# Kernel tuning notes

Hardware: AMD Instinct MI355X
Metric: run time of the kernel (lower is better)

## Reference

```python
import jax, jax.numpy as jnp
import numpy as np

N = 100000   # nodes
E = 600000   # edges per relation
D = 128      # input_dim == output_dim, num_heads = 1
NEG_SLOPE = 0.2  # DGL GATConv default leaky_relu slope


def setup_inputs() -> dict:
    key = jax.random.key(0)
    ks = jax.random.split(key, 10)
    scale = 1.0 / np.sqrt(D)
    return {
        "feat_src": jax.random.normal(ks[0], (N, D), jnp.float32) * 0.1,
        "feat_dst": jax.random.normal(ks[1], (N, D), jnp.float32) * 0.1,
        "intra_src": jax.random.randint(ks[2], (E,), 0, N, jnp.int32),
        "intra_dst": jax.random.randint(ks[3], (E,), 0, N, jnp.int32),
        "inter_src": jax.random.randint(ks[4], (E,), 0, N, jnp.int32),
        "inter_dst": jax.random.randint(ks[5], (E,), 0, N, jnp.int32),
        # 8 GATConvs: conv{1..4} x {intra1, inter}
        "W": jax.random.normal(ks[6], (8, D, D), jnp.float32) * scale,
        "attn_l": jax.random.normal(ks[7], (8, D), jnp.float32) * scale,
        "attn_r": jax.random.normal(ks[8], (8, D), jnp.float32) * scale,
        "bias": jnp.zeros((8, D), jnp.float32),
        "lam": jnp.full((4,), 0.5, jnp.float32),  # lamda1..lamda4
        "n_nodes": N,
    }


def _gat(x_src, x_dst, src, dst, W, al, ar, b, n):
    # DGL GATConv, 1 head, residual=Identity (in==out), no dropout, no activation
    hs = x_src @ W                      # [N, D]
    hd = x_dst @ W                      # [N, D]
    el = hs @ al                        # [N]
    er = hd @ ar                        # [N]
    e = jax.nn.leaky_relu(el[src] + er[dst], NEG_SLOPE)   # [E]
    m = jax.ops.segment_max(e, dst, num_segments=n)
    m = jnp.where(jnp.isfinite(m), m, 0.0)                # empty segments -> 0
    ex = jnp.exp(e - m[dst])
    den = jax.ops.segment_sum(ex, dst, num_segments=n)
    alpha = ex / jnp.maximum(den[dst], 1e-9)              # edge softmax over dst
    agg = jax.ops.segment_sum(alpha[:, None] * hs[src], dst, num_segments=n)
    return agg + x_dst + b              # attention aggregate + residual + bias


def reference(feat_src, feat_dst, intra_src, intra_dst, inter_src, inter_dst,
              W, attn_l, attn_r, bias, lam, n_nodes):
    fwd = ((intra_src, intra_dst), (inter_src, inter_dst))
    rev = ((intra_dst, intra_src), (inter_dst, inter_src))  # g.reverse()

    def conv(xs, xd, edges, i0, i1):
        (s0, d0), (s1, d1) = edges
        # HeteroGraphConv aggregate='sum' over the two relations
        return (_gat(xs, xd, s0, d0, W[i0], attn_l[i0], attn_r[i0], bias[i0], n_nodes)
                + _gat(xs, xd, s1, d1, W[i1], attn_l[i1], attn_r[i1], bias[i1], n_nodes))

    h10 = conv(feat_src, feat_dst, fwd, 0, 1)   # conv1(g, (src, dst))
    h11 = conv(feat_dst, feat_dst, fwd, 2, 3)   # conv2(g, (dst, dst))
    h20 = conv(feat_src, feat_dst, rev, 4, 5)   # conv3(g.rev, (src, dst))
    h21 = conv(feat_dst, feat_dst, rev, 6, 7)   # conv4(g.rev, (dst, dst))

    # hybrid: hl = l1*h10 + l2*h11 ; hr = l3*h20 + l4*h21 ; h = hl + hr
    # head dim is 1 so the max over heads is the identity -> [N, D]
    return lam[0] * h10 + lam[1] * h11 + lam[2] * h20 + lam[3] * h21
```

## Files before the change

kernel.cpp:

```cpp
#include <hip/hip_runtime.h>
#include <hip/hip_bf16.h>

typedef unsigned short ushort_t;
typedef __bf16 bf16x8 __attribute__((ext_vector_type(8)));
typedef ushort_t u16x8 __attribute__((ext_vector_type(8)));
typedef unsigned int u32x4 __attribute__((ext_vector_type(4)));
typedef float f32x4 __attribute__((ext_vector_type(4)));
typedef float f32x2 __attribute__((ext_vector_type(2)));

__device__ __forceinline__ float bf2f(ushort_t u){ return __uint_as_float(((unsigned)u)<<16); }
__device__ __forceinline__ ushort_t f2bf(float f){
  unsigned x = __float_as_uint(f);
  unsigned r = (x + 0x7fffu + ((x>>16)&1u)) >> 16;
  return (ushort_t)r;
}

__global__ __launch_bounds__(256) void init_kernel(const float* __restrict__ W,
    const float* __restrict__ al, const float* __restrict__ ar,
    const float* __restrict__ bias, const float* __restrict__ lam,
    float* __restrict__ wl, float* __restrict__ wr, float* __restrict__ bsum,
    ushort_t* __restrict__ Wf, int* __restrict__ counts, int n) {
  int b = blockIdx.x;
  if (b < 8) {
    int i = b, j = threadIdx.x;
    if (j < 128) {
      const float* Wi  = W + ((size_t)i*128 + j)*128;
      const float* ali = al + i*128;
      const float* ari = ar + i*128;
      float sl = 0.f, sr = 0.f;
      for (int k = 0; k < 128; ++k) { float w = Wi[k]; sl += w*ali[k]; sr += w*ari[k]; }
      wl[i*128+j] = sl; wr[i*128+j] = sr;
      if (i == 0) {
        float bb = 0.f;
        for (int t = 0; t < 8; ++t) bb += lam[t>>1]*bias[t*128+j];
        bsum[j] = bb;
      }
    }
  } else if (b < 72) {
    int tid = (b-8)*256 + threadIdx.x;
    int gat  = tid >> 11;
    int kk   = (tid >> 9) & 3;
    int f    = (tid >> 6) & 7;
    int lane = tid & 63;
    float c = lam[gat >> 1];
    int krow = kk*32 + (lane >> 4)*8;
    int col  = f*16 + (lane & 15);
    ushort_t v[8];
#pragma unroll
    for (int i = 0; i < 8; ++i)
      v[i] = f2bf(c * W[((size_t)gat*128 + krow + i)*128 + col]);
    ushort_t* o = Wf + (size_t)tid*8;
#pragma unroll
    for (int i = 0; i < 8; ++i) o[i] = v[i];
  } else {
    int idx = ((b-72)*256 + threadIdx.x)*4;
    int total = 4*n;
    if (idx + 4 <= total) {
      int4 z = {0,0,0,0};
      *(int4*)(counts + idx) = z;
    } else {
      for (int q = idx; q < total; ++q) counts[q] = 0;
    }
  }
}

__global__ __launch_bounds__(256) void prep_hist_kernel(const float* __restrict__ fs,
    const float* __restrict__ fd, const float* __restrict__ wl, const float* __restrict__ wr,
    float* __restrict__ att, ushort_t* __restrict__ fb,
    const int* __restrict__ ia_s, const int* __restrict__ ia_d,
    const int* __restrict__ ie_s, const int* __restrict__ ie_d,
    int* __restrict__ counts, int n, int e, int n8, int npb, int G) {
  int b = blockIdx.x;
  if (b < npb) {
    int wid  = (b*256 + threadIdx.x) >> 6;
    int lane = threadIdx.x & 63;
    if (wid >= n) return;
    float2 s = *(const float2*)(fs + (size_t)wid*128 + lane*2);
    float2 d = *(const float2*)(fd + (size_t)wid*128 + lane*2);
    ushort2 us; us.x = f2bf(s.x); us.y = f2bf(s.y);
    ushort2 ud; ud.x = f2bf(d.x); ud.y = f2bf(d.y);
    *(ushort2*)(fb + (size_t)wid*256 + lane*2) = us;
    *(ushort2*)(fb + (size_t)wid*256 + 128 + lane*2) = ud;
#pragma unroll
    for (int i = 0; i < 8; ++i) {
      float2 wlv = *(const float2*)(wl + i*128 + lane*2);
      float2 wrv = *(const float2*)(wr + i*128 + lane*2);
      bool use_s = (i==0)||(i==1)||(i==4)||(i==5);
      float xx = use_s ? s.x : d.x;
      float xy = use_s ? s.y : d.y;
      float vl = xx*wlv.x + xy*wlv.y;
      float vr = d.x*wrv.x + d.y*wrv.y;
#pragma unroll
      for (int off = 32; off; off >>= 1) { vl += __shfl_xor(vl, off); vr += __shfl_xor(vr, off); }
      if (lane == 0) { att[(size_t)wid*16 + i] = vl; att[(size_t)wid*16 + 8 + i] = vr; }
    }
  } else {
    int bid = b - npb;
    int x = bid & 7;
    int lo = x*n8, hi = lo + n8; if (hi > n) hi = n;
    int tid = (bid >> 3)*256 + threadIdx.x;
    int nthr = G << 8;
#pragma unroll
    for (int g = 0; g < 4; ++g) {
      const int* dp = (g==0) ? ia_d : (g==1) ? ie_d : (g==2) ? ia_s : ie_s;
      int bo = g*n;
      for (int i = tid*4; i < e; i += nthr*4) {
        if (i + 4 <= e) {
          int4 d4 = *(const int4*)(dp + i);
          if (d4.x >= lo && d4.x < hi) atomicAdd(&counts[bo + d4.x], 1);
          if (d4.y >= lo && d4.y < hi) atomicAdd(&counts[bo + d4.y], 1);
          if (d4.z >= lo && d4.z < hi) atomicAdd(&counts[bo + d4.z], 1);
          if (d4.w >= lo && d4.w < hi) atomicAdd(&counts[bo + d4.w], 1);
        } else {
          for (int q = i; q < e; ++q) {
            int dv = dp[q];
            if (dv >= lo && dv < hi) atomicAdd(&counts[bo + dv], 1);
          }
        }
      }
    }
  }
}

__global__ __launch_bounds__(256) void scan_local_kernel(const int* __restrict__ counts,
    int* __restrict__ rowptr, int* __restrict__ bsums, int total) {
  __shared__ int sh[256];
  int base = blockIdx.x*1024;
  int tid = threadIdx.x;
  int v[4]; int s = 0;
#pragma unroll
  for (int q = 0; q < 4; ++q) { int idx = base + tid*4 + q; int x = (idx < total) ? counts[idx] : 0; v[q] = x; s += x; }
  sh[tid] = s; __syncthreads();
  for (int off = 1; off < 256; off <<= 1) {
    int t2 = (tid >= off) ? sh[tid-off] : 0;
    __syncthreads();
    sh[tid] += t2;
    __syncthreads();
  }
  if (tid == 255) bsums[blockIdx.x] = sh[255];
  int run = sh[tid] - s;
#pragma unroll
  for (int q = 0; q < 4; ++q) { int idx = base + tid*4 + q; if (idx < total) rowptr[idx] = run; run += v[q]; }
}

__global__ __launch_bounds__(512) void scan_finish_kernel(int* __restrict__ rowptr,
    int* __restrict__ cursor, const int* __restrict__ bsums, int total, int nb, int grand) {
  __shared__ int sb[1024];
  __shared__ int ps[512];
  int tid = threadIdx.x;
  int v0 = (2*tid   < nb) ? bsums[2*tid]   : 0;
  int v1 = (2*tid+1 < nb) ? bsums[2*tid+1] : 0;
  int s = v0 + v1;
  ps[tid] = s; __syncthreads();
  for (int off = 1; off < 512; off <<= 1) {
    int t2 = (tid >= off) ? ps[tid-off] : 0;
    __syncthreads();
    ps[tid] += t2;
    __syncthreads();
  }
  int excl = ps[tid] - s;
  sb[2*tid] = excl; sb[2*tid+1] = excl + v0;
  __syncthreads();
  int idx = blockIdx.x*512 + tid;
  if (idx < total) {
    int v = rowptr[idx] + sb[idx >> 10];
    rowptr[idx] = v;
    cursor[idx] = v;
  }
  if (idx == total) rowptr[total] = grand;
}

__global__ __launch_bounds__(256) void fill_kernel(const int* __restrict__ ia_s,
    const int* __restrict__ ia_d, const int* __restrict__ ie_s, const int* __restrict__ ie_d,
    int* __restrict__ cursor, int* __restrict__ col, int n, int e, int n8, int G) {
  int bid = blockIdx.x;
  int x = bid & 7;
  int lo = x*n8, hi = lo + n8; if (hi > n) hi = n;
  int tid = (bid >> 3)*256 + threadIdx.x;
  int nthr = G << 8;
#pragma unroll
  for (int g = 0; g < 4; ++g) {
    const int* dp = (g==0) ? ia_d : (g==1) ? ie_d : (g==2) ? ia_s : ie_s;
    const int* sp = (g==0) ? ia_s : (g==1) ? ie_s : (g==2) ? ia_d : ie_d;
    int bo = g*n;
    for (int i = tid*4; i < e; i += nthr*4) {
      if (i + 4 <= e) {
        int4 d4 = *(const int4*)(dp + i);
        bool m0 = d4.x >= lo && d4.x < hi;
        bool m1 = d4.y >= lo && d4.y < hi;
        bool m2 = d4.z >= lo && d4.z < hi;
        bool m3 = d4.w >= lo && d4.w < hi;
        if (m0 | m1 | m2 | m3) {
          int4 s4 = *(const int4*)(sp + i);
          if (m0) { int pos = atomicAdd(&cursor[bo + d4.x], 1); col[pos] = s4.x; }
          if (m1) { int pos = atomicAdd(&cursor[bo + d4.y], 1); col[pos] = s4.y; }
          if (m2) { int pos = atomicAdd(&cursor[bo + d4.z], 1); col[pos] = s4.z; }
          if (m3) { int pos = atomicAdd(&cursor[bo + d4.w], 1); col[pos] = s4.w; }
        }
      } else {
        for (int q = i; q < e; ++q) {
          int dv = dp[q];
          if (dv >= lo && dv < hi) {
            int pos = atomicAdd(&cursor[bo + dv], 1);
            col[pos] = sp[q];
          }
        }
      }
    }
  }
}

__global__ __launch_bounds__(512) void fused_kernel(const ushort_t* __restrict__ fb,
    const float* __restrict__ att, const int* __restrict__ rowptr,
    const int* __restrict__ col, const ushort_t* __restrict__ Wf,
    const float* __restrict__ lam, const float* __restrict__ bsum,
    float* __restrict__ out, int n) {
  __shared__ ushort_t As[16*1024];
  int t = threadIdx.x, w = t >> 6, lane = t & 63;
  int base = blockIdx.x*16;
  int g = w >> 1;
  int gatA = (g < 2) ? g : g + 2;
  int half = lane >> 5;
  int l    = lane & 31;
  int typ  = (l >> 4) & 1;
  int gat  = gatA + 2*typ;

  for (int i = 0; i < 8; ++i) {
    int di = (w & 1)*8 + i;
    int d = base + di; if (d >= n) d = n - 1;
    int row = rowptr[(size_t)g*n + d], end = rowptr[(size_t)g*n + d + 1];
    float er_ = att[(size_t)d*16 + 8 + gat];
    f32x2 acc0 = {0.f,0.f}, acc1 = {0.f,0.f}, acc2 = {0.f,0.f}, acc3 = {0.f,0.f};
    float den = 0.f;
    int e2 = row + half;
    int sC = 0; float elC = 0.f; u32x4 uC = {0,0,0,0};
    if (e2 < end) {
      sC  = col[e2];
      elC = att[(size_t)sC*16 + gat];
      uC  = *reinterpret_cast<const u32x4*>(fb + (size_t)sC*256 + l*8);
    }
    while (e2 < end) {
      int eN = e2 + 2;
      int sN = sC; float elN = elC; u32x4 uN = uC;
      if (eN < end) {
        sN  = col[eN];
        elN = att[(size_t)sN*16 + gat];
        uN  = *reinterpret_cast<const u32x4*>(fb + (size_t)sN*256 + l*8);
      }
      float ev = elC + er_;
      ev = (ev > 0.f) ? ev : 0.2f*ev;
      float p = __expf(ev);
      den += p;
      f32x2 pv = {p, p};
      f32x2 x0, x1, x2, x3;
      x0[0] = __uint_as_float(uC[0] << 16); x0[1] = __uint_as_float(uC[0] & 0xffff0000u);
      x1[0] = __uint_as_float(uC[1] << 16); x1[1] = __uint_as_float(uC[1] & 0xffff0000u);
      x2[0] = __uint_as_float(uC[2] << 16); x2[1] = __uint_as_float(uC[2] & 0xffff0000u);
      x3[0] = __uint_as_float(uC[3] << 16); x3[1] = __uint_as_float(uC[3] & 0xffff0000u);
      acc0 += pv*x0; acc1 += pv*x1; acc2 += pv*x2; acc3 += pv*x3;
      e2 = eN; sC = sN; elC = elN; uC = uN;
    }
    den += __shfl_xor(den, 32);
    acc0[0] += __shfl_xor(acc0[0], 32); acc0[1] += __shfl_xor(acc0[1], 32);
    acc1[0] += __shfl_xor(acc1[0], 32); acc1[1] += __shfl_xor(acc1[1], 32);
    acc2[0] += __shfl_xor(acc2[0], 32); acc2[1] += __shfl_xor(acc2[1], 32);
    acc3[0] += __shfl_xor(acc3[0], 32); acc3[1] += __shfl_xor(acc3[1], 32);
    if (half == 0) {
      float r = 1.f/fmaxf(den, 1e-9f);
      u16x8 o;
      o[0]=f2bf(acc0[0]*r); o[1]=f2bf(acc0[1]*r); o[2]=f2bf(acc1[0]*r); o[3]=f2bf(acc1[1]*r);
      o[4]=f2bf(acc2[0]*r); o[5]=f2bf(acc2[1]*r); o[6]=f2bf(acc3[0]*r); o[7]=f2bf(acc3[1]*r);
      int k = g*256 + l*8;
      int idx = di*1024 + (k ^ ((di & 7) << 3));
      *reinterpret_cast<u16x8*>(As + idx) = o;
    }
  }
  __syncthreads();

  int lr = lane & 15, lg = lane >> 4;
  f32x4 c0 = {0.f,0.f,0.f,0.f};
#pragma unroll
  for (int ks = 0; ks < 32; ++ks) {
    int kc = ks*32 + lg*8;
    int idx = lr*1024 + (kc ^ ((lr & 7) << 3));
    bf16x8 a = *reinterpret_cast<const bf16x8*>(As + idx);
    int wp = ks >> 3, sub = ks & 7;
    int gg = ((sub >= 4) ? 2 : 0) + ((wp < 2) ? wp : wp + 2);
    int kk = sub & 3;
    const ushort_t* bp = Wf + (((size_t)(gg*4 + kk)*8 + w)*64 + lane)*8;
    bf16x8 b0 = *reinterpret_cast<const bf16x8*>(bp);
    c0 = __builtin_amdgcn_mfma_f32_16x16x32_bf16(a, b0, c0, 0, 0, 0);
  }
  float rc = 2.f*(lam[0] + lam[1] + lam[2] + lam[3]);
  int gc = w*16 + lr;
#pragma unroll
  for (int r2 = 0; r2 < 4; ++r2) {
    int gr = base + lg*4 + r2;
    if (gr < n) {
      size_t o = (size_t)gr*128 + gc;
      float fdv = bf2f(fb[(size_t)gr*256 + 128 + gc]);
      out[o] = c0[r2] + rc*fdv + bsum[gc];
    }
  }
}

extern "C" void kernel_launch(void* const* d_in, const int* in_sizes, int n_in,
                              void* d_out, int out_size, void* d_ws, size_t ws_size,
                              hipStream_t stream) {
  const float* fs  = (const float*)d_in[0];
  const float* fd  = (const float*)d_in[1];
  const int* ia_s  = (const int*)d_in[2];
  const int* ia_d  = (const int*)d_in[3];
  const int* ie_s  = (const int*)d_in[4];
  const int* ie_d  = (const int*)d_in[5];
  const float* W   = (const float*)d_in[6];
  const float* al  = (const float*)d_in[7];
  const float* ar  = (const float*)d_in[8];
  const float* bias= (const float*)d_in[9];
  const float* lam = (const float*)d_in[10];
  int n = in_sizes[0] / 128;
  int e = in_sizes[2];
  float* out = (float*)d_out;

  char* ws = (char*)d_ws;
  size_t off = 0;
  auto alloc = [&](size_t bytes) -> char* { char* p = ws + off; off += (bytes + 255) & ~(size_t)255; return p; };
  float* wl      = (float*)alloc((size_t)8*128*4);
  float* wr      = (float*)alloc((size_t)8*128*4);
  float* bsum    = (float*)alloc(128*4);
  float* att     = (float*)alloc((size_t)n*16*4);
  int*   counts  = (int*)alloc((size_t)4*n*4);
  int*   rowptr  = (int*)alloc(((size_t)4*n + 1)*4);
  int*   bsums   = (int*)alloc(4096);
  int*   colv    = (int*)alloc((size_t)4*e*4);
  ushort_t* Wf   = (ushort_t*)alloc((size_t)8*128*128*2);
  ushort_t* fb   = (ushort_t*)alloc((size_t)n*256*2);
  (void)ws_size; (void)n_in; (void)out_size;

  int n8 = (n + 7)/8;
  int total = 4*n;
  int nb = (total + 1023)/1024;
  int nZ = (total + 1023)/1024;
  int npb = (n + 3)/4;
  int G = 160;

  hipLaunchKernelGGL(init_kernel, dim3(72 + nZ), dim3(256), 0, stream,
                     W, al, ar, bias, lam, wl, wr, bsum, Wf, counts, n);
  hipLaunchKernelGGL(prep_hist_kernel, dim3(npb + 8*G), dim3(256), 0, stream,
                     fs, fd, wl, wr, att, fb, ia_s, ia_d, ie_s, ie_d,
                     counts, n, e, n8, npb, G);
  hipLaunchKernelGGL(scan_local_kernel, dim3(nb), dim3(256), 0, stream,
                     counts, rowptr, bsums, total);
  hipLaunchKernelGGL(scan_finish_kernel, dim3((total + 512)/512), dim3(512), 0, stream,
                     rowptr, counts, bsums, total, nb, 4*e);
  hipLaunchKernelGGL(fill_kernel, dim3(8*G), dim3(256), 0, stream,
                     ia_s, ia_d, ie_s, ie_d, counts, colv, n, e, n8, G);
  hipLaunchKernelGGL(fused_kernel, dim3((n+15)/16), dim3(512), 0, stream,
                     fb, att, rowptr, colv, Wf, lam, bsum, out, n);
}
```

Baseline: 710.3 us.

## Precompute edge attention weights in CSR fill and pack with source index

The CSR fill kernel now computes both leaky-relu-exp attention weights per edge (for the two GATs sharing the edge list), rounds them to bf16, and stores them packed alongside the source index as an int2. The fused aggregation kernel then reads one 8-byte record per edge instead of the column index plus a dependent scattered attention load, and no longer evaluates exp in its inner loop. This removes a dependent gather from the critical aggregation loop. In exchange the fill kernel does more random att reads and writes twice the bytes, and the attention weights lose precision by being stored in bf16.

```diff
diff --git a/kernel.cpp b/kernel.cpp
--- a/kernel.cpp
+++ b/kernel.cpp
@@ -172,7 +172,8 @@
 
 __global__ __launch_bounds__(256) void fill_kernel(const int* __restrict__ ia_s,
     const int* __restrict__ ia_d, const int* __restrict__ ie_s, const int* __restrict__ ie_d,
-    int* __restrict__ cursor, int* __restrict__ col, int n, int e, int n8, int G) {
+    const float* __restrict__ att, int* __restrict__ cursor, int2* __restrict__ epk,
+    int n, int e, int n8, int G) {
   int bid = blockIdx.x;
   int x = bid & 7;
   int lo = x*n8, hi = lo + n8; if (hi > n) hi = n;
@@ -182,9 +183,12 @@
   for (int g = 0; g < 4; ++g) {
     const int* dp = (g==0) ? ia_d : (g==1) ? ie_d : (g==2) ? ia_s : ie_s;
     const int* sp = (g==0) ? ia_s : (g==1) ? ie_s : (g==2) ? ia_d : ie_d;
+    int gatA = (g < 2) ? g : g + 2;
+    int gatB = gatA + 2;
     int bo = g*n;
     for (int i = tid*4; i < e; i += nthr*4) {
-      if (i + 4 <= e) {
+      int lim = (i + 4 <= e) ? 4 : (e - i);
+      if (lim == 4) {
         int4 d4 = *(const int4*)(dp + i);
         bool m0 = d4.x >= lo && d4.x < hi;
         bool m1 = d4.y >= lo && d4.y < hi;
@@ -192,17 +196,35 @@
         bool m3 = d4.w >= lo && d4.w < hi;
         if (m0 | m1 | m2 | m3) {
           int4 s4 = *(const int4*)(sp + i);
-          if (m0) { int pos = atomicAdd(&cursor[bo + d4.x], 1); col[pos] = s4.x; }
-          if (m1) { int pos = atomicAdd(&cursor[bo + d4.y], 1); col[pos] = s4.y; }
-          if (m2) { int pos = atomicAdd(&cursor[bo + d4.z], 1); col[pos] = s4.z; }
-          if (m3) { int pos = atomicAdd(&cursor[bo + d4.w], 1); col[pos] = s4.w; }
+          int dv[4] = {d4.x, d4.y, d4.z, d4.w};
+          int sv[4] = {s4.x, s4.y, s4.z, s4.w};
+          bool mv[4] = {m0, m1, m2, m3};
+#pragma unroll
+          for (int q = 0; q < 4; ++q) {
+            if (mv[q]) {
+              int dd = dv[q], ss = sv[q];
+              float ea = att[(size_t)ss*16 + gatA] + att[(size_t)dd*16 + 8 + gatA];
+              float eb = att[(size_t)ss*16 + gatB] + att[(size_t)dd*16 + 8 + gatB];
+              ea = (ea > 0.f) ? ea : 0.2f*ea;
+              eb = (eb > 0.f) ? eb : 0.2f*eb;
+              unsigned p2 = (unsigned)f2bf(__expf(ea)) | ((unsigned)f2bf(__expf(eb)) << 16);
+              int pos = atomicAdd(&cursor[bo + dd], 1);
+              epk[pos] = make_int2(ss, (int)p2);
+            }
+          }
         }
       } else {
         for (int q = i; q < e; ++q) {
-          int dv = dp[q];
-          if (dv >= lo && dv < hi) {
-            int pos = atomicAdd(&cursor[bo + dv], 1);
-            col[pos] = sp[q];
+          int dd = dp[q];
+          if (dd >= lo && dd < hi) {
+            int ss = sp[q];
+            float ea = att[(size_t)ss*16 + gatA] + att[(size_t)dd*16 + 8 + gatA];
+            float eb = att[(size_t)ss*16 + gatB] + att[(size_t)dd*16 + 8 + gatB];
+            ea = (ea > 0.f) ? ea : 0.2f*ea;
+            eb = (eb > 0.f) ? eb : 0.2f*eb;
+            unsigned p2 = (unsigned)f2bf(__expf(ea)) | ((unsigned)f2bf(__expf(eb)) << 16);
+            int pos = atomicAdd(&cursor[bo + dd], 1);
+            epk[pos] = make_int2(ss, (int)p2);
           }
         }
       }
@@ -211,45 +233,39 @@
 }
 
 __global__ __launch_bounds__(512) void fused_kernel(const ushort_t* __restrict__ fb,
-    const float* __restrict__ att, const int* __restrict__ rowptr,
-    const int* __restrict__ col, const ushort_t* __restrict__ Wf,
-    const float* __restrict__ lam, const float* __restrict__ bsum,
-    float* __restrict__ out, int n) {
+    const int* __restrict__ rowptr, const int2* __restrict__ epk,
+    const ushort_t* __restrict__ Wf, const float* __restrict__ lam,
+    const float* __restrict__ bsum, float* __restrict__ out, int n) {
   __shared__ ushort_t As[16*1024];
   int t = threadIdx.x, w = t >> 6, lane = t & 63;
   int base = blockIdx.x*16;
   int g = w >> 1;
-  int gatA = (g < 2) ? g : g + 2;
   int half = lane >> 5;
   int l    = lane & 31;
   int typ  = (l >> 4) & 1;
-  int gat  = gatA + 2*typ;
 
   for (int i = 0; i < 8; ++i) {
     int di = (w & 1)*8 + i;
     int d = base + di; if (d >= n) d = n - 1;
     int row = rowptr[(size_t)g*n + d], end = rowptr[(size_t)g*n + d + 1];
-    float er_ = att[(size_t)d*16 + 8 + gat];
     f32x2 acc0 = {0.f,0.f}, acc1 = {0.f,0.f}, acc2 = {0.f,0.f}, acc3 = {0.f,0.f};
     float den = 0.f;
     int e2 = row + half;
-    int sC = 0; float elC = 0.f; u32x4 uC = {0,0,0,0};
+    int2 eC = {0, 0}; u32x4 uC = {0,0,0,0};
     if (e2 < end) {
-      sC  = col[e2];
-      elC = att[(size_t)sC*16 + gat];
-      uC  = *reinterpret_cast<const u32x4*>(fb + (size_t)sC*256 + l*8);
+      eC = epk[e2];
+      uC = *reinterpret_cast<const u32x4*>(fb + (size_t)eC.x*256 + l*8);
     }
     while (e2 < end) {
       int eN = e2 + 2;
-      int sN = sC; float elN = elC; u32x4 uN = uC;
+      int2 eT = eC; u32x4 uN = uC;
       if (eN < end) {
-        sN  = col[eN];
-        elN = att[(size_t)sN*16 + gat];
-        uN  = *reinterpret_cast<const u32x4*>(fb + (size_t)sN*256 + l*8);
+        eT = epk[eN];
+        uN = *reinterpret_cast<const u32x4*>(fb + (size_t)eT.x*256 + l*8);
       }
-      float ev = elC + er_;
-      ev = (ev > 0.f) ? ev : 0.2f*ev;
-      float p = __expf(ev);
+      unsigned p2 = (unsigned)eC.y;
+      float p = typ ? __uint_as_float(p2 & 0xffff0000u)
+                    : __uint_as_float(p2 << 16);
       den += p;
       f32x2 pv = {p, p};
       f32x2 x0, x1, x2, x3;
@@ -258,7 +274,7 @@
       x2[0] = __uint_as_float(uC[2] << 16); x2[1] = __uint_as_float(uC[2] & 0xffff0000u);
       x3[0] = __uint_as_float(uC[3] << 16); x3[1] = __uint_as_float(uC[3] & 0xffff0000u);
       acc0 += pv*x0; acc1 += pv*x1; acc2 += pv*x2; acc3 += pv*x3;
-      e2 = eN; sC = sN; elC = elN; uC = uN;
+      e2 = eN; eC = eT; uC = uN;
     }
     den += __shfl_xor(den, 32);
     acc0[0] += __shfl_xor(acc0[0], 32); acc0[1] += __shfl_xor(acc0[1], 32);
@@ -332,7 +348,7 @@
   int*   counts  = (int*)alloc((size_t)4*n*4);
   int*   rowptr  = (int*)alloc(((size_t)4*n + 1)*4);
   int*   bsums   = (int*)alloc(4096);
-  int*   colv    = (int*)alloc((size_t)4*e*4);
+  int2*  epk     = (int2*)alloc((size_t)4*e*8);
   ushort_t* Wf   = (ushort_t*)alloc((size_t)8*128*128*2);
   ushort_t* fb   = (ushort_t*)alloc((size_t)n*256*2);
   (void)ws_size; (void)n_in; (void)out_size;
@@ -354,7 +370,7 @@
   hipLaunchKernelGGL(scan_finish_kernel, dim3((total + 512)/512), dim3(512), 0, stream,
                      rowptr, counts, bsums, total, nb, 4*e);
   hipLaunchKernelGGL(fill_kernel, dim3(8*G), dim3(256), 0, stream,
-                     ia_s, ia_d, ie_s, ie_d, counts, colv, n, e, n8, G);
+                     ia_s, ia_d, ie_s, ie_d, att, counts, epk, n, e, n8, G);
   hipLaunchKernelGGL(fused_kernel, dim3((n+15)/16), dim3(512), 0, stream,
-                     fb, att, rowptr, colv, Wf, lam, bsum, out, n);
-}
+                     fb, rowptr, epk, Wf, lam, bsum, out, n);
+}
```

Result: no change. 706.1 us (-0.6%).
